# Optimization experiments

Measured on AMD Instinct MI355X. Metric: run time of the kernel, lower is better.

The kernel has to match this reference:

```python
import jax, jax.numpy as jnp
import numpy as np

D_MODEL = 1024
N_HEADS = 16
D_K = D_MODEL // N_HEADS
B, L = 4, 2048


def setup_inputs() -> dict:
    key = jax.random.key(0)
    ks = jax.random.split(key, 9)
    s = 1.0 / np.sqrt(D_MODEL)
    return {
        "x": jax.random.normal(ks[0], (B, L, D_MODEL), dtype=jnp.float32),
        "mask": jnp.ones((B, L), dtype=jnp.int32),
        "Wq": jax.random.uniform(ks[1], (D_MODEL, D_MODEL), jnp.float32, -s, s),
        "bq": jax.random.uniform(ks[2], (D_MODEL,), jnp.float32, -s, s),
        "Wk": jax.random.uniform(ks[3], (D_MODEL, D_MODEL), jnp.float32, -s, s),
        "bk": jax.random.uniform(ks[4], (D_MODEL,), jnp.float32, -s, s),
        "Wv": jax.random.uniform(ks[5], (D_MODEL, D_MODEL), jnp.float32, -s, s),
        "bv": jax.random.uniform(ks[6], (D_MODEL,), jnp.float32, -s, s),
        "Wo": jax.random.uniform(ks[7], (D_MODEL, D_MODEL), jnp.float32, -s, s),
        "bo": jax.random.uniform(ks[8], (D_MODEL,), jnp.float32, -s, s),
    }


def reference(x, mask, Wq, bq, Wk, bk, Wv, bv, Wo, bo):
    b, l, d = x.shape
    # project and split heads: [B, H, L, d_k]
    def heads(W, bias):
        return (x @ W.T + bias).reshape(b, l, N_HEADS, D_K).transpose(0, 2, 1, 3)
    Q = heads(Wq, bq)
    K = heads(Wk, bk)
    V = heads(Wv, bv)
    scores = jnp.einsum("bhqd,bhkd->bhqk", Q, K) / np.sqrt(D_K).astype(np.float32)
    # mask: [B, L] -> broadcast over heads and query dim as [B, 1, 1, L]
    scores = jnp.where(mask[:, None, None, :] == 0, jnp.float32(-1e9), scores)
    attn = jax.nn.softmax(scores, axis=-1)  # dropout=0 in eval math
    out = jnp.einsum("bhqk,bhkd->bhqd", attn, V)
    out = out.transpose(0, 2, 1, 3).reshape(b, l, d)
    return out @ Wo.T + bo
```

## Files before the change

kernel.cpp:

```cpp
#include <hip/hip_runtime.h>
#include <stdint.h>

#define DMODEL 1024
#define NHEADS 16
#define DK     64
#define BATCH  4
#define SEQ    2048
#define MROWS  (BATCH*SEQ)

typedef __bf16   bf16x8 __attribute__((ext_vector_type(8)));
typedef float    f32x4  __attribute__((ext_vector_type(4)));
typedef _Float16 f16x4  __attribute__((ext_vector_type(4)));

#if defined(__has_builtin)
#if __has_builtin(__builtin_amdgcn_exp2f)
#define EXP2F(x) __builtin_amdgcn_exp2f(x)
#endif
#endif
#ifndef EXP2F
#define EXP2F(x) exp2f(x)
#endif

__device__ __forceinline__ unsigned short f2bf(float f) {
    unsigned int u = __builtin_bit_cast(unsigned int, f);
    u += 0x7fffu + ((u >> 16) & 1u);
    return (unsigned short)(u >> 16);
}

__device__ __forceinline__ unsigned int pack_bf16(float a, float b) {
    unsigned int ua = __builtin_bit_cast(unsigned int, a) + 0x8000u;
    unsigned int ub = __builtin_bit_cast(unsigned int, b) + 0x8000u;
    return __builtin_amdgcn_perm(ub, ua, 0x07060302u);
}
__device__ __forceinline__ unsigned int pack_f16(float a, float b) {
    return __builtin_bit_cast(unsigned int, __builtin_amdgcn_cvt_pkrtz(a, b));
}

#define GLDS(gp, lp) __builtin_amdgcn_global_load_lds( \
    (const __attribute__((address_space(1))) unsigned int*)(gp), \
    (__attribute__((address_space(3))) unsigned int*)(lp), 16, 0, 0)

__global__ void cvt_kernel(const float* __restrict__ src,
                           unsigned short* __restrict__ dst, int n4) {
    int i = blockIdx.x * blockDim.x + threadIdx.x;
    if (i >= n4) return;
    const float4 v = reinterpret_cast<const float4*>(src)[i];
    uint2 o;
    o.x = pack_bf16(v.x, v.y);
    o.y = pack_bf16(v.z, v.w);
    reinterpret_cast<uint2*>(dst)[i] = o;
}

__global__ void cvtw_kernel(const float* __restrict__ w0, const float* __restrict__ w1,
                            const float* __restrict__ w2, const float* __restrict__ w3,
                            unsigned short* __restrict__ d0, unsigned short* __restrict__ d1,
                            unsigned short* __restrict__ d2, unsigned short* __restrict__ d3) {
    const float* s; unsigned short* d;
    switch (blockIdx.y) {
        case 0:  s = w0; d = d0; break;
        case 1:  s = w1; d = d1; break;
        case 2:  s = w2; d = d2; break;
        default: s = w3; d = d3; break;
    }
    const int i = blockIdx.x * blockDim.x + threadIdx.x;
    const float4 v = reinterpret_cast<const float4*>(s)[i];
    uint2 o;
    o.x = pack_bf16(v.x, v.y);
    o.y = pack_bf16(v.z, v.w);
    reinterpret_cast<uint2*>(d)[i] = o;
}

__global__ void maskbias_kernel(const int* __restrict__ m, float* __restrict__ o, int n) {
    const int i = blockIdx.x * blockDim.x + threadIdx.x;
    if (i < n) o[i] = m[i] ? 0.f : -1e30f;
}

template<int MODE>
__global__ __launch_bounds__(256, 4) void gemm128(
        const unsigned short* __restrict__ A,
        const unsigned short* __restrict__ W0,
        const unsigned short* __restrict__ W1,
        const unsigned short* __restrict__ W2,
        const float* __restrict__ b0,
        const float* __restrict__ b1,
        const float* __restrict__ b2,
        void* __restrict__ o0, void* __restrict__ o1, void* __restrict__ o2) {
    __shared__ unsigned short As[128 * 64];
    __shared__ unsigned short Bs[128 * 64];
    const int lane = threadIdx.x & 63;
    const int wave = threadIdx.x >> 6;
    const int quad = lane >> 4;
    const int r15  = lane & 15;
    const int wr = wave >> 1, wc = wave & 1;
    const int m0 = blockIdx.y * 128;

    int which, ncol0;
    const unsigned short* W;
    const float* bias;
    if (MODE == 0) {
        which = blockIdx.x >> 3;
        ncol0 = (blockIdx.x & 7) * 128;
        W    = which == 0 ? W0 : (which == 1 ? W1 : W2);
        bias = which == 0 ? b0 : (which == 1 ? b1 : b2);
    } else {
        which = 0; ncol0 = blockIdx.x * 128; W = W0; bias = b0;
    }

    const int srow = lane >> 3;
    const int scg  = (lane & 7) ^ srow;
    const unsigned short* Ag[4];
    const unsigned short* Wg[4];
    #pragma unroll
    for (int j = 0; j < 4; ++j) {
        const int row = (wave * 4 + j) * 8 + srow;
        Ag[j] = A + (m0 + row) * DMODEL + scg * 8;
        Wg[j] = W + (ncol0 + row) * DMODEL + scg * 8;
    }

    f32x4 acc[4][4] = {};
    for (int kk = 0; kk < DMODEL; kk += 64) {
        __syncthreads();
        #pragma unroll
        for (int j = 0; j < 4; ++j) {
            GLDS(Ag[j] + kk, &As[(wave * 4 + j) * 512]);
            GLDS(Wg[j] + kk, &Bs[(wave * 4 + j) * 512]);
        }
        __syncthreads();
        #pragma unroll
        for (int u = 0; u < 2; ++u) {
            bf16x8 af[4], bfx[4];
            const int cs = ((u * 4 + quad) ^ (r15 & 7)) * 8;
            #pragma unroll
            for (int t = 0; t < 4; ++t) {
                af[t]  = *(const bf16x8*)&As[(wr * 64 + t * 16 + r15) * 64 + cs];
                bfx[t] = *(const bf16x8*)&Bs[(wc * 64 + t * 16 + r15) * 64 + cs];
            }
            #pragma unroll
            for (int mt = 0; mt < 4; ++mt)
                #pragma unroll
                for (int nt = 0; nt < 4; ++nt)
                    acc[mt][nt] = __builtin_amdgcn_mfma_f32_16x16x32_bf16(
                        af[mt], bfx[nt], acc[mt][nt], 0, 0, 0);
        }
    }

    if (MODE == 1) {
        #pragma unroll
        for (int mt = 0; mt < 4; ++mt) {
            #pragma unroll
            for (int nt = 0; nt < 4; ++nt) {
                const int row0 = m0 + wr * 64 + mt * 16 + quad * 4;
                const int col  = ncol0 + wc * 64 + nt * 16 + r15;
                const float bb = bias[col];
                #pragma unroll
                for (int r = 0; r < 4; ++r)
                    ((float*)o0)[(size_t)(row0 + r) * DMODEL + col] = acc[mt][nt][r] + bb;
            }
        }
        return;
    }

    __syncthreads();
    unsigned short* Ts = (wave < 2) ? &As[wave * 4096] : &Bs[(wave - 2) * 4096];
    char* const Tb = (char*)Ts;

    const int b_idx = m0 >> 11;
    const int h     = (ncol0 >> 6) + wc;
    const int l0    = (m0 & (SEQ - 1)) + wr * 64;

    if (which == 2) {
        #pragma unroll
        for (int nt = 0; nt < 4; ++nt) {
            const float bb = bias[ncol0 + wc * 64 + nt * 16 + r15];
            const int drow = nt * 16 + r15;
            #pragma unroll
            for (int mt = 0; mt < 4; ++mt) {
                const int sw = (mt * 2 + (quad >> 1)) ^ (r15 & 7);
                uint2 pw;
                pw.x = pack_f16(acc[mt][nt][0] + bb, acc[mt][nt][1] + bb);
                pw.y = pack_f16(acc[mt][nt][2] + bb, acc[mt][nt][3] + bb);
                *(uint2*)(Tb + drow * 128 + sw * 16 + (quad & 1) * 8) = pw;
            }
        }
        _Float16* gout = (_Float16*)o2
            + (size_t)(b_idx * NHEADS + h) * (SEQ * DK) + (size_t)(l0 >> 6) * (DK * 64);
        #pragma unroll
        for (int seg = 0; seg < 8; ++seg) {
            const uint4 vv = *(const uint4*)(Tb + seg * 1024
                + (lane >> 3) * 128 + (((lane & 7) ^ (lane >> 3)) * 16));
            *(uint4*)(gout + seg * 512 + lane * 8) = vv;
        }
    } else {
        #pragma unroll
        for (int nt = 0; nt < 4; ++nt) {
            const float bb = bias[ncol0 + wc * 64 + nt * 16 + r15];
            const int dloc = nt * 16 + r15;
            const int chb  = dloc >> 3;
            const int dby  = (dloc & 7) * 2;
            #pragma unroll
            for (int mt = 0; mt < 4; ++mt) {
                #pragma unroll
                for (int r = 0; r < 4; ++r) {
                    const int lloc = mt * 16 + quad * 4 + r;
                    float v = acc[mt][nt][r] + bb;
                    if (which == 0) v *= 0.18033688011112042f;
                    const int sw = chb ^ (lloc & 7);
                    *(unsigned short*)(Tb + lloc * 128 + sw * 16 + dby) = f2bf(v);
                }
            }
        }
        unsigned short* ow = (unsigned short*)(which == 0 ? o0 : o1);
        unsigned short* gout = ow + ((size_t)(b_idx * NHEADS + h) * SEQ + l0) * DK;
        #pragma unroll
        for (int seg = 0; seg < 8; ++seg) {
            const uint4 vv = *(const uint4*)(Tb + seg * 1024
                + (lane >> 3) * 128 + (((lane & 7) ^ (lane >> 3)) * 16));
            *(uint4*)(gout + seg * 512 + lane * 8) = vv;
        }
    }
}

__global__ __launch_bounds__(256, 4) void flash_attn(
        const unsigned short* __restrict__ Q,
        const unsigned short* __restrict__ Km,
        const unsigned short* __restrict__ Vm,
        const float* __restrict__ mbf,
        unsigned short* __restrict__ Oa) {
    __shared__ unsigned short Ks[64 * 64];
    __shared__ unsigned short Vs[64 * 64];
    const int lane = threadIdx.x & 63;
    const int wave = threadIdx.x >> 6;
    const int quad = lane >> 4;
    const int r15  = lane & 15;

    const int id   = (blockIdx.y << 4) | blockIdx.x;
    const int xcd  = id & 7;
    const int slot = id >> 3;
    const int bh   = xcd + ((slot >> 4) << 3);
    const int qt   = slot & 15;
    const int b = bh >> 4, h = bh & (NHEADS - 1);
    const int q0 = qt * 128 + wave * 32;

    const unsigned short* Qb = Q  + (size_t)bh * SEQ * DK;
    const unsigned short* Kb = Km + (size_t)bh * SEQ * DK;
    const unsigned short* Vb = Vm + (size_t)bh * SEQ * DK;
    const float* mb = mbf + b * SEQ;

    const int srow = lane >> 3;
    const int soff = (srow * 64) + (((lane & 7) ^ srow) * 8);

    bf16x8 bq[2][2];
    #pragma unroll
    for (int qf = 0; qf < 2; ++qf)
        #pragma unroll
        for (int u = 0; u < 2; ++u)
            bq[qf][u] = *(const bf16x8*)(Qb + (q0 + qf * 16 + r15) * DK + u * 32 + quad * 8);

    float l_part[2] = {0.f, 0.f};
    f32x4 oacc[2][4] = {};

    for (int kb = 0; kb < SEQ; kb += 64) {
        __syncthreads();
        const unsigned short* Kg = Kb + kb * 64;
        const unsigned short* Vg = Vb + kb * 64;
        #pragma unroll
        for (int j = 0; j < 2; ++j) {
            const int wseg = wave * 2 + j;
            GLDS(Kg + wseg * 512 + soff, &Ks[wseg * 512]);
            GLDS(Vg + wseg * 512 + soff, &Vs[wseg * 512]);
        }
        __syncthreads();

        f16x4 pfrag[4][2];
        #pragma unroll
        for (int t = 0; t < 4; ++t) {
            const bf16x8 ak0 = *(const bf16x8*)&Ks[(t * 16 + r15) * 64 + ((quad ^ (r15 & 7)) * 8)];
            const bf16x8 ak1 = *(const bf16x8*)&Ks[(t * 16 + r15) * 64 + (((4 + quad) ^ (r15 & 7)) * 8)];
            const float4 m4 = *(const float4*)(mb + kb + t * 16 + quad * 4);
            #pragma unroll
            for (int qf = 0; qf < 2; ++qf) {
                f32x4 z = {};
                z = __builtin_amdgcn_mfma_f32_16x16x32_bf16(ak0, bq[qf][0], z, 0, 0, 0);
                z = __builtin_amdgcn_mfma_f32_16x16x32_bf16(ak1, bq[qf][1], z, 0, 0, 0);
                const float p0 = EXP2F(z[0] + m4.x);
                const float p1 = EXP2F(z[1] + m4.y);
                const float p2 = EXP2F(z[2] + m4.z);
                const float p3 = EXP2F(z[3] + m4.w);
                l_part[qf] += (p0 + p1) + (p2 + p3);
                uint2 pw;
                pw.x = pack_f16(p0, p1);
                pw.y = pack_f16(p2, p3);
                pfrag[t][qf] = __builtin_bit_cast(f16x4, pw);
            }
        }

        #pragma unroll
        for (int nt = 0; nt < 4; ++nt) {
            #pragma unroll
            for (int t = 0; t < 4; ++t) {
                const int chunk = (2 * t + (quad >> 1)) ^ (r15 & 7);
                const f16x4 vf = *(const f16x4*)&Vs[(nt * 16 + r15) * 64 + chunk * 8 + (quad & 1) * 4];
                #pragma unroll
                for (int qf = 0; qf < 2; ++qf)
                    oacc[qf][nt] = __builtin_amdgcn_mfma_f32_16x16x16f16(
                        vf, pfrag[t][qf], oacc[qf][nt], 0, 0, 0);
            }
        }
    }

    #pragma unroll
    for (int qf = 0; qf < 2; ++qf) {
        float l = l_part[qf];
        l += __shfl_xor(l, 16);
        l += __shfl_xor(l, 32);
        const float rl = __builtin_amdgcn_rcpf(l);
        const int row = q0 + qf * 16 + r15;
        #pragma unroll
        for (int nt = 0; nt < 4; ++nt) {
            const int col0 = h * DK + nt * 16 + quad * 4;
            uint2 pw;
            pw.x = pack_bf16(oacc[qf][nt][0] * rl, oacc[qf][nt][1] * rl);
            pw.y = pack_bf16(oacc[qf][nt][2] * rl, oacc[qf][nt][3] * rl);
            *(uint2*)&Oa[((size_t)b * SEQ + row) * DMODEL + col0] = pw;
        }
    }
}

extern "C" void kernel_launch(void* const* d_in, const int* in_sizes, int n_in,
                              void* d_out, int out_size, void* d_ws, size_t ws_size,
                              hipStream_t stream) {
    (void)in_sizes; (void)n_in; (void)out_size; (void)ws_size;
    const float* x  = (const float*)d_in[0];
    const int* mask = (const int*)d_in[1];
    const float* Wq = (const float*)d_in[2];
    const float* bq = (const float*)d_in[3];
    const float* Wk = (const float*)d_in[4];
    const float* bk = (const float*)d_in[5];
    const float* Wv = (const float*)d_in[6];
    const float* bv = (const float*)d_in[7];
    const float* Wo = (const float*)d_in[8];
    const float* bo = (const float*)d_in[9];
    float* out = (float*)d_out;

    char* ws = (char*)d_ws;
    unsigned short* xb  = (unsigned short*)(ws);
    unsigned short* wqb = (unsigned short*)(ws + 16777216);
    unsigned short* wkb = (unsigned short*)(ws + 16777216 + 1 * 2097152);
    unsigned short* wvb = (unsigned short*)(ws + 16777216 + 2 * 2097152);
    unsigned short* wob = (unsigned short*)(ws + 16777216 + 3 * 2097152);
    unsigned short* qb  = (unsigned short*)(ws + 16777216 + 4 * 2097152);
    unsigned short* kb  = qb  + (size_t)MROWS * DMODEL;
    unsigned short* vtb = kb  + (size_t)MROWS * DMODEL;
    unsigned short* ab  = vtb + (size_t)MROWS * DMODEL;
    float*          mbf = (float*)(ab + (size_t)MROWS * DMODEL);

    cvt_kernel<<<dim3(MROWS * DMODEL / 4 / 256), 256, 0, stream>>>(x, xb, MROWS * DMODEL / 4);
    cvtw_kernel<<<dim3(DMODEL * DMODEL / 4 / 256, 4), 256, 0, stream>>>(
        Wq, Wk, Wv, Wo, wqb, wkb, wvb, wob);
    maskbias_kernel<<<dim3(BATCH * SEQ / 256), 256, 0, stream>>>(mask, mbf, BATCH * SEQ);

    gemm128<0><<<dim3(24, MROWS / 128), 256, 0, stream>>>(
        xb, wqb, wkb, wvb, bq, bk, bv, qb, kb, vtb);

    flash_attn<<<dim3(16, BATCH * NHEADS), 256, 0, stream>>>(qb, kb, vtb, mbf, ab);

    gemm128<1><<<dim3(8, MROWS / 128), 256, 0, stream>>>(
        ab, wob, nullptr, nullptr, bo, nullptr, nullptr, out, nullptr, nullptr);
}
```

Before: 325.3 us.

## Double-buffer K/V tiles in flash attention and add all-valid mask fast path

The attention loop now keeps two LDS buffers for K and V. Each iteration prefetches the next 64-key tile while computing on the current one, so only one barrier per iteration remains and global-to-LDS loads can overlap the MFMA and exp work. The mask kernel also records, per 64-key block, whether every mask entry is nonzero. The attention kernel uses that flag to skip the mask-bias load and adds on fully valid blocks. In exchange, LDS use per block doubles and the branch adds some code size.

```diff
diff --git a/kernel.cpp b/kernel.cpp
--- a/kernel.cpp
+++ b/kernel.cpp
@@ -70,9 +70,17 @@
     reinterpret_cast<uint2*>(d)[i] = o;
 }
 
-__global__ void maskbias_kernel(const int* __restrict__ m, float* __restrict__ o, int n) {
+__global__ void maskbias_kernel(const int* __restrict__ m, float* __restrict__ o,
+                                int* __restrict__ avb, int n) {
     const int i = blockIdx.x * blockDim.x + threadIdx.x;
     if (i < n) o[i] = m[i] ? 0.f : -1e30f;
+    if (i < n / 64) {
+        const int* g = m + i * 64;
+        int all = 1;
+        #pragma unroll 8
+        for (int j = 0; j < 64; ++j) all &= (g[j] != 0);
+        avb[i] = all;
+    }
 }
 
 template<int MODE>
@@ -225,9 +233,10 @@
         const unsigned short* __restrict__ Km,
         const unsigned short* __restrict__ Vm,
         const float* __restrict__ mbf,
+        const int* __restrict__ avb,
         unsigned short* __restrict__ Oa) {
-    __shared__ unsigned short Ks[64 * 64];
-    __shared__ unsigned short Vs[64 * 64];
+    __shared__ unsigned short Ks[2][64 * 64];
+    __shared__ unsigned short Vs[2][64 * 64];
     const int lane = threadIdx.x & 63;
     const int wave = threadIdx.x >> 6;
     const int quad = lane >> 4;
@@ -245,6 +254,7 @@
     const unsigned short* Kb = Km + (size_t)bh * SEQ * DK;
     const unsigned short* Vb = Vm + (size_t)bh * SEQ * DK;
     const float* mb = mbf + b * SEQ;
+    const int*   av = avb + b * (SEQ / 64);
 
     const int srow = lane >> 3;
     const int soff = (srow * 64) + (((lane & 7) ^ srow) * 8);
@@ -259,38 +269,72 @@
     float l_part[2] = {0.f, 0.f};
     f32x4 oacc[2][4] = {};
 
-    for (int kb = 0; kb < SEQ; kb += 64) {
+    {
+        const int wseg = wave * 2;
+        GLDS(Kb + wseg * 512 + soff, &Ks[0][wseg * 512]);
+        GLDS(Kb + (wseg + 1) * 512 + soff, &Ks[0][(wseg + 1) * 512]);
+        GLDS(Vb + wseg * 512 + soff, &Vs[0][wseg * 512]);
+        GLDS(Vb + (wseg + 1) * 512 + soff, &Vs[0][(wseg + 1) * 512]);
+    }
+
+    int cur = 0;
+    for (int kb = 0; kb < SEQ; kb += 64, cur ^= 1) {
         __syncthreads();
-        const unsigned short* Kg = Kb + kb * 64;
-        const unsigned short* Vg = Vb + kb * 64;
-        #pragma unroll
-        for (int j = 0; j < 2; ++j) {
-            const int wseg = wave * 2 + j;
-            GLDS(Kg + wseg * 512 + soff, &Ks[wseg * 512]);
-            GLDS(Vg + wseg * 512 + soff, &Vs[wseg * 512]);
-        }
-        __syncthreads();
+        if (kb + 64 < SEQ) {
+            const unsigned short* Kg = Kb + (kb + 64) * 64;
+            const unsigned short* Vg = Vb + (kb + 64) * 64;
+            const int wseg = wave * 2;
+            GLDS(Kg + wseg * 512 + soff, &Ks[cur ^ 1][wseg * 512]);
+            GLDS(Kg + (wseg + 1) * 512 + soff, &Ks[cur ^ 1][(wseg + 1) * 512]);
+            GLDS(Vg + wseg * 512 + soff, &Vs[cur ^ 1][wseg * 512]);
+            GLDS(Vg + (wseg + 1) * 512 + soff, &Vs[cur ^ 1][(wseg + 1) * 512]);
+        }
+        const unsigned short* const Kc = Ks[cur];
+        const unsigned short* const Vc = Vs[cur];
 
         f16x4 pfrag[4][2];
-        #pragma unroll
-        for (int t = 0; t < 4; ++t) {
-            const bf16x8 ak0 = *(const bf16x8*)&Ks[(t * 16 + r15) * 64 + ((quad ^ (r15 & 7)) * 8)];
-            const bf16x8 ak1 = *(const bf16x8*)&Ks[(t * 16 + r15) * 64 + (((4 + quad) ^ (r15 & 7)) * 8)];
-            const float4 m4 = *(const float4*)(mb + kb + t * 16 + quad * 4);
-            #pragma unroll
-            for (int qf = 0; qf < 2; ++qf) {
-                f32x4 z = {};
-                z = __builtin_amdgcn_mfma_f32_16x16x32_bf16(ak0, bq[qf][0], z, 0, 0, 0);
-                z = __builtin_amdgcn_mfma_f32_16x16x32_bf16(ak1, bq[qf][1], z, 0, 0, 0);
-                const float p0 = EXP2F(z[0] + m4.x);
-                const float p1 = EXP2F(z[1] + m4.y);
-                const float p2 = EXP2F(z[2] + m4.z);
-                const float p3 = EXP2F(z[3] + m4.w);
-                l_part[qf] += (p0 + p1) + (p2 + p3);
-                uint2 pw;
-                pw.x = pack_f16(p0, p1);
-                pw.y = pack_f16(p2, p3);
-                pfrag[t][qf] = __builtin_bit_cast(f16x4, pw);
+        if (av[kb >> 6]) {
+            #pragma unroll
+            for (int t = 0; t < 4; ++t) {
+                const bf16x8 ak0 = *(const bf16x8*)&Kc[(t * 16 + r15) * 64 + ((quad ^ (r15 & 7)) * 8)];
+                const bf16x8 ak1 = *(const bf16x8*)&Kc[(t * 16 + r15) * 64 + (((4 + quad) ^ (r15 & 7)) * 8)];
+                #pragma unroll
+                for (int qf = 0; qf < 2; ++qf) {
+                    f32x4 z = {};
+                    z = __builtin_amdgcn_mfma_f32_16x16x32_bf16(ak0, bq[qf][0], z, 0, 0, 0);
+                    z = __builtin_amdgcn_mfma_f32_16x16x32_bf16(ak1, bq[qf][1], z, 0, 0, 0);
+                    const float p0 = EXP2F(z[0]);
+                    const float p1 = EXP2F(z[1]);
+                    const float p2 = EXP2F(z[2]);
+                    const float p3 = EXP2F(z[3]);
+                    l_part[qf] += (p0 + p1) + (p2 + p3);
+                    uint2 pw;
+                    pw.x = pack_f16(p0, p1);
+                    pw.y = pack_f16(p2, p3);
+                    pfrag[t][qf] = __builtin_bit_cast(f16x4, pw);
+                }
+            }
+        } else {
+            #pragma unroll
+            for (int t = 0; t < 4; ++t) {
+                const bf16x8 ak0 = *(const bf16x8*)&Kc[(t * 16 + r15) * 64 + ((quad ^ (r15 & 7)) * 8)];
+                const bf16x8 ak1 = *(const bf16x8*)&Kc[(t * 16 + r15) * 64 + (((4 + quad) ^ (r15 & 7)) * 8)];
+                const float4 m4 = *(const float4*)(mb + kb + t * 16 + quad * 4);
+                #pragma unroll
+                for (int qf = 0; qf < 2; ++qf) {
+                    f32x4 z = {};
+                    z = __builtin_amdgcn_mfma_f32_16x16x32_bf16(ak0, bq[qf][0], z, 0, 0, 0);
+                    z = __builtin_amdgcn_mfma_f32_16x16x32_bf16(ak1, bq[qf][1], z, 0, 0, 0);
+                    const float p0 = EXP2F(z[0] + m4.x);
+                    const float p1 = EXP2F(z[1] + m4.y);
+                    const float p2 = EXP2F(z[2] + m4.z);
+                    const float p3 = EXP2F(z[3] + m4.w);
+                    l_part[qf] += (p0 + p1) + (p2 + p3);
+                    uint2 pw;
+                    pw.x = pack_f16(p0, p1);
+                    pw.y = pack_f16(p2, p3);
+                    pfrag[t][qf] = __builtin_bit_cast(f16x4, pw);
+                }
             }
         }
 
@@ -299,7 +343,7 @@
             #pragma unroll
             for (int t = 0; t < 4; ++t) {
                 const int chunk = (2 * t + (quad >> 1)) ^ (r15 & 7);
-                const f16x4 vf = *(const f16x4*)&Vs[(nt * 16 + r15) * 64 + chunk * 8 + (quad & 1) * 4];
+                const f16x4 vf = *(const f16x4*)&Vc[(nt * 16 + r15) * 64 + chunk * 8 + (quad & 1) * 4];
                 #pragma unroll
                 for (int qf = 0; qf < 2; ++qf)
                     oacc[qf][nt] = __builtin_amdgcn_mfma_f32_16x16x16f16(
@@ -353,16 +397,17 @@
     unsigned short* vtb = kb  + (size_t)MROWS * DMODEL;
     unsigned short* ab  = vtb + (size_t)MROWS * DMODEL;
     float*          mbf = (float*)(ab + (size_t)MROWS * DMODEL);
+    int*            avb = (int*)(mbf + MROWS);
 
     cvt_kernel<<<dim3(MROWS * DMODEL / 4 / 256), 256, 0, stream>>>(x, xb, MROWS * DMODEL / 4);
     cvtw_kernel<<<dim3(DMODEL * DMODEL / 4 / 256, 4), 256, 0, stream>>>(
         Wq, Wk, Wv, Wo, wqb, wkb, wvb, wob);
-    maskbias_kernel<<<dim3(BATCH * SEQ / 256), 256, 0, stream>>>(mask, mbf, BATCH * SEQ);
+    maskbias_kernel<<<dim3(BATCH * SEQ / 256), 256, 0, stream>>>(mask, mbf, avb, BATCH * SEQ);
 
     gemm128<0><<<dim3(24, MROWS / 128), 256, 0, stream>>>(
         xb, wqb, wkb, wvb, bq, bk, bv, qb, kb, vtb);
 
-    flash_attn<<<dim3(16, BATCH * NHEADS), 256, 0, stream>>>(qb, kb, vtb, mbf, ab);
+    flash_attn<<<dim3(16, BATCH * NHEADS), 256, 0, stream>>>(qb, kb, vtb, mbf, avb, ab);
 
     gemm128<1><<<dim3(8, MROWS / 128), 256, 0, stream>>>(
         ab, wob, nullptr, nullptr, bo, nullptr, nullptr, out, nullptr, nullptr);
```

Measured after the change: 325.8 us. Within noise of the previous version (+0.2%).
